# Kernel tuning notes

Measured on AMD Instinct MI355X. Metric: run time of the kernel, lower is better.

Reference implementation:

```python
import jax, jax.numpy as jnp
import numpy as np

N = 8192
F_DIM = 512
H_DIM = 256


def _xavier(key, shape):
    fan_in, fan_out = shape
    limit = float(np.sqrt(6.0 / (fan_in + fan_out)))
    return jax.random.uniform(key, shape, jnp.float32, -limit, limit)


def setup_inputs() -> dict:
    key = jax.random.key(0)
    k1, k2, k3, k4, k5, k6, k7 = jax.random.split(key, 7)
    inp = {
        "input": jax.random.normal(k1, (N, F_DIM), jnp.float32),
        "wavelets": jax.random.normal(k2, (N, N), jnp.float32) / np.sqrt(N),
        "wavelets_inv": jax.random.normal(k3, (N, N), jnp.float32) / np.sqrt(N),
        "W1": _xavier(k4, (F_DIM, H_DIM)),
        "W2": _xavier(k5, (H_DIM, H_DIM)),
        "filter1": jax.random.uniform(k6, (N,), jnp.float32, 0.9, 1.1),
        "filter2": jax.random.uniform(k7, (N,), jnp.float32, 0.9, 1.1),
    }
    return inp


def _gwnn_layer(x, wavelets, wavelets_inv, weight, filt):
    # torch: wavelets @ diag(filt) @ (wavelets_inv @ (x @ W))
    # diag(filt) right-multiply == column-wise scale of wavelets (same math,
    # avoids the O(N^3) dense diag matmul).
    t = x @ weight                      # [N, C_out]
    s = wavelets_inv @ t                # [N, C_out] (spectral domain)
    return (wavelets * filt[None, :]) @ s  # [N, C_out]


def reference(input, wavelets, wavelets_inv, W1, W2, filter1, filter2):
    # eval mode: dropout is identity
    h1 = jax.nn.relu(_gwnn_layer(input, wavelets, wavelets_inv, W1, filter1))
    out = _gwnn_layer(h1, wavelets, wavelets_inv, W2, filter2)
    return out
```

## Files before the change

kernel.cpp:

```cpp
#include <hip/hip_runtime.h>
#include <hip/hip_bf16.h>

using f32x4 = __attribute__((ext_vector_type(4))) float;
using s16x8 = __attribute__((ext_vector_type(8))) short;

#define DEVFN static __device__ __forceinline__

static constexpr int NCOL = 256;
static constexpr int MROWS = 8192;
static constexpr int BM = 64;
static constexpr int BK = 128;
static constexpr int THREADS = 512;
static constexpr int NTILE = MROWS / BM;

DEVFN unsigned short f2bf(float f) {
  union { float f; unsigned u; } x; x.f = f;
  unsigned u = x.u;
  u += 0x7fffu + ((u >> 16) & 1u);
  return (unsigned short)(u >> 16);
}

DEVFN s16x8 pack8(f32x4 v0, f32x4 v1) {
  union { s16x8 v; __hip_bfloat162 h[4]; } pk;
  pk.h[0] = __float22bfloat162_rn(float2{v0[0], v0[1]});
  pk.h[1] = __float22bfloat162_rn(float2{v0[2], v0[3]});
  pk.h[2] = __float22bfloat162_rn(float2{v1[0], v1[1]});
  pk.h[3] = __float22bfloat162_rn(float2{v1[2], v1[3]});
  return pk.v;
}

DEVFN void async16(void* lds, const void* g) {
  __builtin_amdgcn_global_load_lds((const __attribute__((address_space(1))) unsigned*)g,
                                   (__attribute__((address_space(3))) unsigned*)lds,
                                   16, 0, 0);
}

template<bool ABLK, int KS, bool WB>
__global__ __launch_bounds__(THREADS, 4)
void gemm_m(const void* __restrict__ Aany, int Kfull,
            const unsigned short* __restrict__ Bp8,
            float* __restrict__ Cpart, unsigned short* __restrict__ Awb)
{
  __shared__ __align__(16) unsigned short As[2][BM * BK];

  const int nwg = NTILE * KS, q = nwg / 8;
  const int logical = (blockIdx.x & 7) * q + (blockIdx.x >> 3);
  const int kh = logical >> 7;
  const int tile = logical & 127;
  const int klen = Kfull / KS;
  const int nt = klen / BK;
  const int k0 = kh * klen;
  const int tid = threadIdx.x, lane = tid & 63;
  const int wm = (tid >> 6) >> 2;
  const int wn = (tid >> 6) & 3;
  const int lr = lane & 15, lg = lane >> 4;
  const int srow = tid >> 3, sseg = tid & 7;

  const float* Af32 = (const float*)Aany;
  const unsigned short* Abf = (const unsigned short*)Aany;
  const int ktiles = Kfull >> 7;

  f32x4 rv[4];
  auto loadA = [&](int t) {
    const float* p = Af32 + (size_t)(tile * BM + srow) * Kfull + k0 + t * BK + sseg * 16;
    rv[0] = *(const f32x4*)p;       rv[1] = *(const f32x4*)(p + 4);
    rv[2] = *(const f32x4*)(p + 8); rv[3] = *(const f32x4*)(p + 12);
  };
  auto putA = [&](int buf, int t) {
    s16x8 p0 = pack8(rv[0], rv[1]), p1 = pack8(rv[2], rv[3]);
    const int kc0 = sseg * 2;
    *(s16x8*)&As[buf][srow * 128 + (((kc0    ) ^ (srow & 15)) << 3)] = p0;
    *(s16x8*)&As[buf][srow * 128 + (((kc0 + 1) ^ (srow & 15)) << 3)] = p1;
    if constexpr (WB) {
      unsigned short* w = Awb + ((size_t)tile * ktiles + (k0 >> 7) + t) * 8192
                        + srow * 128 + sseg * 16;
      *(s16x8*)w = p0; *(s16x8*)(w + 8) = p1;
    }
  };
  auto stageBf = [&](int buf, int t) {
    const unsigned short* base = Abf + ((size_t)tile * ktiles + (k0 >> 7) + t) * 8192;
#pragma unroll
    for (int o = 0; o < 2; ++o) {
      const int bs = o * 8192 + tid * 16;
      const int row = bs >> 8, ch = (bs >> 4) & 15;
      async16(&As[buf][o * 4096 + tid * 8], base + row * 128 + ((ch ^ (row & 15)) << 3));
    }
  };

  const unsigned short* bptr = Bp8 + ((size_t)(k0 >> 3) + lg) * 2048
                             + (size_t)(wn * 64 + lr) * 8;
  s16x8 bb[2][4];
  auto ldb = [&](const unsigned short* p, s16x8* d) {
#pragma unroll
    for (int fn = 0; fn < 4; ++fn) d[fn] = *(const s16x8*)(p + fn * 128);
  };

  f32x4 acc[2][4] = {};

  if constexpr (ABLK) { stageBf(0, 0); } else { loadA(0); putA(0, 0); }
  ldb(bptr, bb[0]);
  bptr += 8192;
  __syncthreads();

  int cur = 0;
  for (int t = 0; t < nt; ++t) {
    const bool pre = (t + 1 < nt);
    if (pre) { if constexpr (ABLK) stageBf(cur ^ 1, t + 1); else loadA(t + 1); }
#pragma unroll
    for (int s = 0; s < 4; ++s) {
      if (pre || s < 3) { ldb(bptr, bb[(s + 1) & 1]); bptr += 8192; }
      s16x8 a0, a1;
      {
        const int r0 = wm * 32 + lr, kc = s * 4 + lg;
        a0 = *(const s16x8*)&As[cur][r0 * 128 + ((kc ^ (r0 & 15)) << 3)];
        const int r1 = r0 + 16;
        a1 = *(const s16x8*)&As[cur][r1 * 128 + ((kc ^ (r1 & 15)) << 3)];
      }
#pragma unroll
      for (int fn = 0; fn < 4; ++fn) {
        acc[0][fn] = __builtin_amdgcn_mfma_f32_16x16x32_bf16(a0, bb[s & 1][fn], acc[0][fn], 0, 0, 0);
        acc[1][fn] = __builtin_amdgcn_mfma_f32_16x16x32_bf16(a1, bb[s & 1][fn], acc[1][fn], 0, 0, 0);
      }
    }
    if constexpr (!ABLK) { if (pre) putA(cur ^ 1, t + 1); }
    __syncthreads();
    cur ^= 1;
  }

  float* Co = Cpart + (size_t)kh * MROWS * NCOL;
#pragma unroll
  for (int fm = 0; fm < 2; ++fm) {
    const int row = tile * BM + wm * 32 + fm * 16 + lg * 4;
#pragma unroll
    for (int fn = 0; fn < 4; ++fn) {
      const int col = wn * 64 + fn * 16 + lr;
#pragma unroll
      for (int r = 0; r < 4; ++r)
        Co[(size_t)(row + r) * NCOL + col] = acc[fm][fn][r];
    }
  }
}


__global__ void k_convert_p8(const float* __restrict__ W, int K,
                             unsigned short* __restrict__ outp) {
  int tid = blockIdx.x * blockDim.x + threadIdx.x;
  if (tid >= K * NCOL / 4) return;
  int j = tid & (NCOL - 1);
  int i0 = (tid >> 8) << 2;
  unsigned short u[4];
#pragma unroll
  for (int r = 0; r < 4; ++r) u[r] = f2bf(W[(size_t)(i0 + r) * NCOL + j]);
  size_t off = ((size_t)(i0 >> 3) * NCOL + j) * 8 + (i0 & 7);
  *(ushort4*)&outp[off] = make_ushort4(u[0], u[1], u[2], u[3]);
}

template<int NS, int MODE>
__global__ void k_reduce(const float* __restrict__ P, const float* __restrict__ filt,
                         void* __restrict__ Out) {
  int tid = blockIdx.x * blockDim.x + threadIdx.x;
  if constexpr (MODE == 0) {
    int j = tid & (NCOL - 1);
    int i0 = (tid >> 8) << 2;
    unsigned short u[4];
#pragma unroll
    for (int r = 0; r < 4; ++r) {
      size_t o = (size_t)(i0 + r) * NCOL + j;
      float v = 0.f;
#pragma unroll
      for (int h = 0; h < NS; ++h) v += P[(size_t)h * MROWS * NCOL + o];
      if (filt) v *= filt[i0 + r];
      u[r] = f2bf(v);
    }
    size_t off = ((size_t)(i0 >> 3) * NCOL + j) * 8 + (i0 & 7);
    *(ushort4*)&((unsigned short*)Out)[off] = make_ushort4(u[0], u[1], u[2], u[3]);
  } else {
    size_t o = (size_t)tid * 4;
    float4 v = *(const float4*)&P[o];
#pragma unroll
    for (int h = 1; h < NS; ++h) {
      float4 b = *(const float4*)&P[(size_t)h * MROWS * NCOL + o];
      v.x += b.x; v.y += b.y; v.z += b.z; v.w += b.w;
    }
    if constexpr (MODE == 1) {
      const int m = (int)(o >> 8), c = (int)(o & 255);
      ushort4 u;
      u.x = f2bf(fmaxf(v.x, 0.f)); u.y = f2bf(fmaxf(v.y, 0.f));
      u.z = f2bf(fmaxf(v.z, 0.f)); u.w = f2bf(fmaxf(v.w, 0.f));
      size_t off = ((size_t)(m >> 6) * 2 + (c >> 7)) * 8192 + (m & 63) * 128 + (c & 127);
      *(ushort4*)&((unsigned short*)Out)[off] = u;
    } else {
      *(float4*)&((float*)Out)[o] = v;
    }
  }
}

extern "C" void kernel_launch(void* const* d_in, const int* in_sizes, int n_in,
                              void* d_out, int out_size, void* d_ws, size_t ws_size,
                              hipStream_t stream) {
  const float* input = (const float*)d_in[0];
  const float* Wv    = (const float*)d_in[1];
  const float* Winv  = (const float*)d_in[2];
  const float* W1    = (const float*)d_in[3];
  const float* W2    = (const float*)d_in[4];
  const float* f1    = (const float*)d_in[5];
  const float* f2    = (const float*)d_in[6];
  float* out = (float*)d_out;

  char* ws = (char*)d_ws;
  unsigned short* WvB   = (unsigned short*)(ws);
  unsigned short* WinvB = (unsigned short*)(ws + 0x8000000);
  float* part           = (float*)(ws + 0x10000000);
  unsigned short* t1p   = (unsigned short*)(ws + 0x12000000);
  unsigned short* s1p   = (unsigned short*)(ws + 0x12400000);
  unsigned short* t2p   = (unsigned short*)(ws + 0x12800000);
  unsigned short* s2p   = (unsigned short*)(ws + 0x12C00000);
  unsigned short* h1b   = (unsigned short*)(ws + 0x13000000);
  unsigned short* W1p   = (unsigned short*)(ws + 0x13400000);
  unsigned short* W2p   = (unsigned short*)(ws + 0x13440000);

  dim3 gT(THREADS);
  dim3 g4(NTILE * 4), g2(NTILE * 2);
  dim3 rT(256), rG(MROWS * NCOL / 4 / 256);

  k_convert_p8<<<dim3(128), rT, 0, stream>>>(W1, 512, W1p);
  k_convert_p8<<<dim3(64),  rT, 0, stream>>>(W2, 256, W2p);

  gemm_m<false, 4, false><<<g4, gT, 0, stream>>>((const void*)input, 512, W1p, part, nullptr);
  k_reduce<4, 0><<<rG, rT, 0, stream>>>(part, nullptr, t1p);
  gemm_m<false, 4, true><<<g4, gT, 0, stream>>>((const void*)Winv, 8192, t1p, part, WinvB);
  k_reduce<4, 0><<<rG, rT, 0, stream>>>(part, f1, s1p);
  gemm_m<false, 4, true><<<g4, gT, 0, stream>>>((const void*)Wv, 8192, s1p, part, WvB);
  k_reduce<4, 1><<<rG, rT, 0, stream>>>(part, nullptr, h1b);
  gemm_m<true, 2, false><<<g2, gT, 0, stream>>>((const void*)h1b, 256, W2p, part, nullptr);
  k_reduce<2, 0><<<rG, rT, 0, stream>>>(part, nullptr, t2p);
  gemm_m<true, 4, false><<<g4, gT, 0, stream>>>((const void*)WinvB, 8192, t2p, part, nullptr);
  k_reduce<4, 0><<<rG, rT, 0, stream>>>(part, f2, s2p);
  gemm_m<true, 4, false><<<g4, gT, 0, stream>>>((const void*)WvB, 8192, s2p, part, nullptr);
  k_reduce<4, 2><<<rG, rT, 0, stream>>>(part, nullptr, out);
}
```

Measured before the change: 430.2 us.

## Double K tile depth to 256 and split fp32 A staging in halves

Raises the GEMM K tile from 128 to 256, so each block does twice as many MFMA steps per barrier and the LDS swizzle widens to 32 chunks. The fp32 A path now loads and converts in two halves interleaved with the MFMA steps, which keeps register pressure down and overlaps the global loads with compute. The blocked bf16 layouts for the cached wavelets and h1 change to 256-wide tiles, and the small W1/W2 GEMMs use fewer K splits. LDS use doubles to 64KB per block, which may cut occupancy.

Result: slower. 497.2 us (+15.6%).

```diff
diff --git a/kernel.cpp b/kernel.cpp
--- a/kernel.cpp
+++ b/kernel.cpp
@@ -9,7 +9,7 @@
 static constexpr int NCOL = 256;
 static constexpr int MROWS = 8192;
 static constexpr int BM = 64;
-static constexpr int BK = 128;
+static constexpr int BK = 256;
 static constexpr int THREADS = 512;
 static constexpr int NTILE = MROWS / BM;
 
@@ -58,32 +58,34 @@
 
   const float* Af32 = (const float*)Aany;
   const unsigned short* Abf = (const unsigned short*)Aany;
-  const int ktiles = Kfull >> 7;
+  const int ktiles = Kfull >> 8;
 
   f32x4 rv[4];
-  auto loadA = [&](int t) {
-    const float* p = Af32 + (size_t)(tile * BM + srow) * Kfull + k0 + t * BK + sseg * 16;
+  auto loadA_h = [&](int t, int h) {
+    const float* p = Af32 + (size_t)(tile * BM + srow) * Kfull
+                   + k0 + t * BK + sseg * 32 + h * 16;
     rv[0] = *(const f32x4*)p;       rv[1] = *(const f32x4*)(p + 4);
     rv[2] = *(const f32x4*)(p + 8); rv[3] = *(const f32x4*)(p + 12);
   };
-  auto putA = [&](int buf, int t) {
+  auto putA_h = [&](int buf, int t, int h) {
     s16x8 p0 = pack8(rv[0], rv[1]), p1 = pack8(rv[2], rv[3]);
-    const int kc0 = sseg * 2;
-    *(s16x8*)&As[buf][srow * 128 + (((kc0    ) ^ (srow & 15)) << 3)] = p0;
-    *(s16x8*)&As[buf][srow * 128 + (((kc0 + 1) ^ (srow & 15)) << 3)] = p1;
+    const int c0 = sseg * 4 + h * 2;
+    *(s16x8*)&As[buf][srow * 256 + (((c0    ) ^ (srow & 31)) << 3)] = p0;
+    *(s16x8*)&As[buf][srow * 256 + (((c0 + 1) ^ (srow & 31)) << 3)] = p1;
     if constexpr (WB) {
-      unsigned short* w = Awb + ((size_t)tile * ktiles + (k0 >> 7) + t) * 8192
-                        + srow * 128 + sseg * 16;
+      unsigned short* w = Awb + ((size_t)tile * ktiles + (k0 >> 8) + t) * 16384
+                        + srow * 256 + sseg * 32 + h * 16;
       *(s16x8*)w = p0; *(s16x8*)(w + 8) = p1;
     }
   };
   auto stageBf = [&](int buf, int t) {
-    const unsigned short* base = Abf + ((size_t)tile * ktiles + (k0 >> 7) + t) * 8192;
-#pragma unroll
-    for (int o = 0; o < 2; ++o) {
-      const int bs = o * 8192 + tid * 16;
-      const int row = bs >> 8, ch = (bs >> 4) & 15;
-      async16(&As[buf][o * 4096 + tid * 8], base + row * 128 + ((ch ^ (row & 15)) << 3));
+    const unsigned short* base = Abf + ((size_t)tile * ktiles + (k0 >> 8) + t) * 16384;
+#pragma unroll
+    for (int o = 0; o < 4; ++o) {
+      const int slot = o * 8192 + tid * 16;
+      const int row = slot >> 9, ch = (slot >> 4) & 31;
+      async16(&As[buf][o * 4096 + tid * 8],
+              base + row * 256 + ((ch ^ (row & 31)) << 3));
     }
   };
 
@@ -97,32 +99,39 @@
 
   f32x4 acc[2][4] = {};
 
-  if constexpr (ABLK) { stageBf(0, 0); } else { loadA(0); putA(0, 0); }
-  ldb(bptr, bb[0]);
-  bptr += 8192;
+  if constexpr (ABLK) {
+    stageBf(0, 0);
+  } else {
+    loadA_h(0, 0); putA_h(0, 0, 0);
+    loadA_h(0, 1); putA_h(0, 0, 1);
+  }
+  ldb(bptr, bb[0]); bptr += 8192;
   __syncthreads();
 
   int cur = 0;
   for (int t = 0; t < nt; ++t) {
     const bool pre = (t + 1 < nt);
-    if (pre) { if constexpr (ABLK) stageBf(cur ^ 1, t + 1); else loadA(t + 1); }
-#pragma unroll
-    for (int s = 0; s < 4; ++s) {
-      if (pre || s < 3) { ldb(bptr, bb[(s + 1) & 1]); bptr += 8192; }
+    if (pre) { if constexpr (ABLK) stageBf(cur ^ 1, t + 1); else loadA_h(t + 1, 0); }
+#pragma unroll
+    for (int s = 0; s < 8; ++s) {
+      if (s < 7 || pre) { ldb(bptr, bb[(s + 1) & 1]); bptr += 8192; }
       s16x8 a0, a1;
       {
         const int r0 = wm * 32 + lr, kc = s * 4 + lg;
-        a0 = *(const s16x8*)&As[cur][r0 * 128 + ((kc ^ (r0 & 15)) << 3)];
+        a0 = *(const s16x8*)&As[cur][r0 * 256 + ((kc ^ (r0 & 31)) << 3)];
         const int r1 = r0 + 16;
-        a1 = *(const s16x8*)&As[cur][r1 * 128 + ((kc ^ (r1 & 15)) << 3)];
+        a1 = *(const s16x8*)&As[cur][r1 * 256 + ((kc ^ (r1 & 31)) << 3)];
       }
 #pragma unroll
       for (int fn = 0; fn < 4; ++fn) {
         acc[0][fn] = __builtin_amdgcn_mfma_f32_16x16x32_bf16(a0, bb[s & 1][fn], acc[0][fn], 0, 0, 0);
         acc[1][fn] = __builtin_amdgcn_mfma_f32_16x16x32_bf16(a1, bb[s & 1][fn], acc[1][fn], 0, 0, 0);
       }
-    }
-    if constexpr (!ABLK) { if (pre) putA(cur ^ 1, t + 1); }
+      if constexpr (!ABLK) {
+        if (pre && s == 3) { putA_h(cur ^ 1, t + 1, 0); loadA_h(t + 1, 1); }
+        if (pre && s == 6) { putA_h(cur ^ 1, t + 1, 1); }
+      }
+    }
     __syncthreads();
     cur ^= 1;
   }
@@ -187,7 +196,7 @@
       ushort4 u;
       u.x = f2bf(fmaxf(v.x, 0.f)); u.y = f2bf(fmaxf(v.y, 0.f));
       u.z = f2bf(fmaxf(v.z, 0.f)); u.w = f2bf(fmaxf(v.w, 0.f));
-      size_t off = ((size_t)(m >> 6) * 2 + (c >> 7)) * 8192 + (m & 63) * 128 + (c & 127);
+      size_t off = (size_t)(m >> 6) * 16384 + (m & 63) * 256 + c;
       *(ushort4*)&((unsigned short*)Out)[off] = u;
     } else {
       *(float4*)&((float*)Out)[o] = v;
@@ -220,20 +229,20 @@
   unsigned short* W2p   = (unsigned short*)(ws + 0x13440000);
 
   dim3 gT(THREADS);
-  dim3 g4(NTILE * 4), g2(NTILE * 2);
+  dim3 g4(NTILE * 4), g2(NTILE * 2), g1(NTILE);
   dim3 rT(256), rG(MROWS * NCOL / 4 / 256);
 
   k_convert_p8<<<dim3(128), rT, 0, stream>>>(W1, 512, W1p);
   k_convert_p8<<<dim3(64),  rT, 0, stream>>>(W2, 256, W2p);
 
-  gemm_m<false, 4, false><<<g4, gT, 0, stream>>>((const void*)input, 512, W1p, part, nullptr);
-  k_reduce<4, 0><<<rG, rT, 0, stream>>>(part, nullptr, t1p);
+  gemm_m<false, 2, false><<<g2, gT, 0, stream>>>((const void*)input, 512, W1p, part, nullptr);
+  k_reduce<2, 0><<<rG, rT, 0, stream>>>(part, nullptr, t1p);
   gemm_m<false, 4, true><<<g4, gT, 0, stream>>>((const void*)Winv, 8192, t1p, part, WinvB);
   k_reduce<4, 0><<<rG, rT, 0, stream>>>(part, f1, s1p);
   gemm_m<false, 4, true><<<g4, gT, 0, stream>>>((const void*)Wv, 8192, s1p, part, WvB);
   k_reduce<4, 1><<<rG, rT, 0, stream>>>(part, nullptr, h1b);
-  gemm_m<true, 2, false><<<g2, gT, 0, stream>>>((const void*)h1b, 256, W2p, part, nullptr);
-  k_reduce<2, 0><<<rG, rT, 0, stream>>>(part, nullptr, t2p);
+  gemm_m<true, 1, false><<<g1, gT, 0, stream>>>((const void*)h1b, 256, W2p, part, nullptr);
+  k_reduce<1, 0><<<rG, rT, 0, stream>>>(part, nullptr, t2p);
   gemm_m<true, 4, false><<<g4, gT, 0, stream>>>((const void*)WinvB, 8192, t2p, part, nullptr);
   k_reduce<4, 0><<<rG, rT, 0, stream>>>(part, f2, s2p);
   gemm_m<true, 4, false><<<g4, gT, 0, stream>>>((const void*)WvB, 8192, s2p, part, nullptr);
```

## Pre-convert A matrices to blocked bf16 and stage B through LDS asynchronously

Applied to the files above, without the earlier changes.

Adds dedicated conversion kernels that turn Wv, Winv and the input into swizzled 64x64 bf16 blocks before any GEMM, so every GEMM streams bf16 A tiles with async global-to-LDS loads. B tiles are now also staged into LDS asynchronously instead of being read per-wave from global into registers, and BK drops to 64. The small GEMMs (x@W1, h1@W2) run without K-split and write packed bf16 output directly, which removes two reduce launches. The cost is two extra full passes over the 8192x8192 matrices as standalone conversions, where before the conversion was fused into the first GEMMs that read them, plus a larger LDS footprint that may reduce occupancy.

Result: faster. 410.8 us (-4.5%).

```diff
diff --git a/kernel.cpp b/kernel.cpp
--- a/kernel.cpp
+++ b/kernel.cpp
@@ -9,7 +9,7 @@
 static constexpr int NCOL = 256;
 static constexpr int MROWS = 8192;
 static constexpr int BM = 64;
-static constexpr int BK = 128;
+static constexpr int BK = 64;
 static constexpr int THREADS = 512;
 static constexpr int NTILE = MROWS / BM;
 
@@ -35,112 +35,107 @@
                                    16, 0, 0);
 }
 
-template<bool ABLK, int KS, bool WB>
+
+template<int KS, int EPI>
 __global__ __launch_bounds__(THREADS, 4)
-void gemm_m(const void* __restrict__ Aany, int Kfull,
+void gemm_b(const unsigned short* __restrict__ Ablk, int Kfull,
             const unsigned short* __restrict__ Bp8,
-            float* __restrict__ Cpart, unsigned short* __restrict__ Awb)
+            float* __restrict__ Cpart, unsigned short* __restrict__ Pout)
 {
   __shared__ __align__(16) unsigned short As[2][BM * BK];
+  __shared__ __align__(16) unsigned short Bs[2][BK * NCOL];
 
   const int nwg = NTILE * KS, q = nwg / 8;
   const int logical = (blockIdx.x & 7) * q + (blockIdx.x >> 3);
-  const int kh = logical >> 7;
-  const int tile = logical & 127;
+  const int kh = logical / NTILE;
+  const int tile = logical % NTILE;
   const int klen = Kfull / KS;
   const int nt = klen / BK;
   const int k0 = kh * klen;
+  const int KT = Kfull >> 6;
   const int tid = threadIdx.x, lane = tid & 63;
   const int wm = (tid >> 6) >> 2;
   const int wn = (tid >> 6) & 3;
   const int lr = lane & 15, lg = lane >> 4;
-  const int srow = tid >> 3, sseg = tid & 7;
-
-  const float* Af32 = (const float*)Aany;
-  const unsigned short* Abf = (const unsigned short*)Aany;
-  const int ktiles = Kfull >> 7;
-
-  f32x4 rv[4];
-  auto loadA = [&](int t) {
-    const float* p = Af32 + (size_t)(tile * BM + srow) * Kfull + k0 + t * BK + sseg * 16;
-    rv[0] = *(const f32x4*)p;       rv[1] = *(const f32x4*)(p + 4);
-    rv[2] = *(const f32x4*)(p + 8); rv[3] = *(const f32x4*)(p + 12);
+
+  auto stage = [&](int buf, int t) {
+    const unsigned short* asrc = Ablk + ((size_t)tile * KT + (k0 >> 6) + t) * 4096 + tid * 8;
+    async16(&As[buf][tid * 8], asrc);
+    const unsigned short* bsrc = Bp8 + (size_t)(k0 + t * BK) * NCOL + tid * 8;
+#pragma unroll
+    for (int o = 0; o < 4; ++o)
+      async16(&Bs[buf][o * 4096 + tid * 8], bsrc + o * 4096);
   };
-  auto putA = [&](int buf, int t) {
-    s16x8 p0 = pack8(rv[0], rv[1]), p1 = pack8(rv[2], rv[3]);
-    const int kc0 = sseg * 2;
-    *(s16x8*)&As[buf][srow * 128 + (((kc0    ) ^ (srow & 15)) << 3)] = p0;
-    *(s16x8*)&As[buf][srow * 128 + (((kc0 + 1) ^ (srow & 15)) << 3)] = p1;
-    if constexpr (WB) {
-      unsigned short* w = Awb + ((size_t)tile * ktiles + (k0 >> 7) + t) * 8192
-                        + srow * 128 + sseg * 16;
-      *(s16x8*)w = p0; *(s16x8*)(w + 8) = p1;
-    }
-  };
-  auto stageBf = [&](int buf, int t) {
-    const unsigned short* base = Abf + ((size_t)tile * ktiles + (k0 >> 7) + t) * 8192;
-#pragma unroll
-    for (int o = 0; o < 2; ++o) {
-      const int bs = o * 8192 + tid * 16;
-      const int row = bs >> 8, ch = (bs >> 4) & 15;
-      async16(&As[buf][o * 4096 + tid * 8], base + row * 128 + ((ch ^ (row & 15)) << 3));
-    }
-  };
-
-  const unsigned short* bptr = Bp8 + ((size_t)(k0 >> 3) + lg) * 2048
-                             + (size_t)(wn * 64 + lr) * 8;
-  s16x8 bb[2][4];
-  auto ldb = [&](const unsigned short* p, s16x8* d) {
-#pragma unroll
-    for (int fn = 0; fn < 4; ++fn) d[fn] = *(const s16x8*)(p + fn * 128);
-  };
 
   f32x4 acc[2][4] = {};
 
-  if constexpr (ABLK) { stageBf(0, 0); } else { loadA(0); putA(0, 0); }
-  ldb(bptr, bb[0]);
-  bptr += 8192;
+  stage(0, 0);
   __syncthreads();
 
   int cur = 0;
   for (int t = 0; t < nt; ++t) {
-    const bool pre = (t + 1 < nt);
-    if (pre) { if constexpr (ABLK) stageBf(cur ^ 1, t + 1); else loadA(t + 1); }
-#pragma unroll
-    for (int s = 0; s < 4; ++s) {
-      if (pre || s < 3) { ldb(bptr, bb[(s + 1) & 1]); bptr += 8192; }
-      s16x8 a0, a1;
-      {
-        const int r0 = wm * 32 + lr, kc = s * 4 + lg;
-        a0 = *(const s16x8*)&As[cur][r0 * 128 + ((kc ^ (r0 & 15)) << 3)];
-        const int r1 = r0 + 16;
-        a1 = *(const s16x8*)&As[cur][r1 * 128 + ((kc ^ (r1 & 15)) << 3)];
+    if (t + 1 < nt) stage(cur ^ 1, t + 1);
+#pragma unroll
+    for (int s = 0; s < 2; ++s) {
+      const int kc = s * 4 + lg;
+      const int r0 = wm * 32 + lr, r1 = r0 + 16;
+      s16x8 a0 = *(const s16x8*)&As[cur][r0 * 64 + ((kc ^ (r0 & 7)) << 3)];
+      s16x8 a1 = *(const s16x8*)&As[cur][r1 * 64 + ((kc ^ (r1 & 7)) << 3)];
+#pragma unroll
+      for (int fn = 0; fn < 4; ++fn) {
+        s16x8 b = *(const s16x8*)&Bs[cur][kc * 2048 + (wn * 64 + fn * 16 + lr) * 8];
+        acc[0][fn] = __builtin_amdgcn_mfma_f32_16x16x32_bf16(a0, b, acc[0][fn], 0, 0, 0);
+        acc[1][fn] = __builtin_amdgcn_mfma_f32_16x16x32_bf16(a1, b, acc[1][fn], 0, 0, 0);
       }
-#pragma unroll
-      for (int fn = 0; fn < 4; ++fn) {
-        acc[0][fn] = __builtin_amdgcn_mfma_f32_16x16x32_bf16(a0, bb[s & 1][fn], acc[0][fn], 0, 0, 0);
-        acc[1][fn] = __builtin_amdgcn_mfma_f32_16x16x32_bf16(a1, bb[s & 1][fn], acc[1][fn], 0, 0, 0);
-      }
-    }
-    if constexpr (!ABLK) { if (pre) putA(cur ^ 1, t + 1); }
+    }
     __syncthreads();
     cur ^= 1;
   }
 
-  float* Co = Cpart + (size_t)kh * MROWS * NCOL;
-#pragma unroll
-  for (int fm = 0; fm < 2; ++fm) {
-    const int row = tile * BM + wm * 32 + fm * 16 + lg * 4;
-#pragma unroll
-    for (int fn = 0; fn < 4; ++fn) {
-      const int col = wn * 64 + fn * 16 + lr;
-#pragma unroll
-      for (int r = 0; r < 4; ++r)
-        Co[(size_t)(row + r) * NCOL + col] = acc[fm][fn][r];
+  if constexpr (EPI == 0) {
+    float* Co = Cpart + (size_t)kh * MROWS * NCOL;
+#pragma unroll
+    for (int fm = 0; fm < 2; ++fm) {
+      const int row = tile * BM + wm * 32 + fm * 16 + lg * 4;
+#pragma unroll
+      for (int fn = 0; fn < 4; ++fn) {
+        const int col = wn * 64 + fn * 16 + lr;
+#pragma unroll
+        for (int r = 0; r < 4; ++r)
+          Co[(size_t)(row + r) * NCOL + col] = acc[fm][fn][r];
+      }
+    }
+  } else {
+#pragma unroll
+    for (int fm = 0; fm < 2; ++fm) {
+      const int r0 = tile * BM + wm * 32 + fm * 16 + lg * 4;
+#pragma unroll
+      for (int fn = 0; fn < 4; ++fn) {
+        const int col = wn * 64 + fn * 16 + lr;
+        ushort4 u;
+        u.x = f2bf(acc[fm][fn][0]); u.y = f2bf(acc[fm][fn][1]);
+        u.z = f2bf(acc[fm][fn][2]); u.w = f2bf(acc[fm][fn][3]);
+        *(ushort4*)&Pout[((size_t)(r0 >> 3) * 256 + col) * 8 + (r0 & 7)] = u;
+      }
     }
   }
 }
 
+
+template<int KTSH>
+__global__ void k_cvt_ablk(const float* __restrict__ W, unsigned short* __restrict__ outp) {
+  const int K = 64 << KTSH;
+  size_t gid = (size_t)blockIdx.x * blockDim.x + threadIdx.x;
+  const int k8 = (int)(gid & 7);
+  const size_t rr = gid >> 3;
+  const int row = (int)(rr & 63);
+  const size_t bt = rr >> 6;
+  const int t = (int)(bt & ((1 << KTSH) - 1));
+  const size_t T = bt >> KTSH;
+  const float* p = W + (T * 64 + row) * (size_t)K + t * 64 + k8 * 8;
+  s16x8 v = pack8(*(const f32x4*)p, *(const f32x4*)(p + 4));
+  *(s16x8*)&outp[bt * 4096 + row * 64 + ((k8 ^ (row & 7)) << 3)] = v;
+}
 
 __global__ void k_convert_p8(const float* __restrict__ W, int K,
                              unsigned short* __restrict__ outp) {
@@ -155,7 +150,7 @@
   *(ushort4*)&outp[off] = make_ushort4(u[0], u[1], u[2], u[3]);
 }
 
-template<int NS, int MODE>
+template<int MODE>
 __global__ void k_reduce(const float* __restrict__ P, const float* __restrict__ filt,
                          void* __restrict__ Out) {
   int tid = blockIdx.x * blockDim.x + threadIdx.x;
@@ -166,9 +161,8 @@
 #pragma unroll
     for (int r = 0; r < 4; ++r) {
       size_t o = (size_t)(i0 + r) * NCOL + j;
-      float v = 0.f;
-#pragma unroll
-      for (int h = 0; h < NS; ++h) v += P[(size_t)h * MROWS * NCOL + o];
+      float v = P[o] + P[(size_t)MROWS * NCOL + o]
+              + P[2 * (size_t)MROWS * NCOL + o] + P[3 * (size_t)MROWS * NCOL + o];
       if (filt) v *= filt[i0 + r];
       u[r] = f2bf(v);
     }
@@ -176,18 +170,19 @@
     *(ushort4*)&((unsigned short*)Out)[off] = make_ushort4(u[0], u[1], u[2], u[3]);
   } else {
     size_t o = (size_t)tid * 4;
-    float4 v = *(const float4*)&P[o];
-#pragma unroll
-    for (int h = 1; h < NS; ++h) {
-      float4 b = *(const float4*)&P[(size_t)h * MROWS * NCOL + o];
-      v.x += b.x; v.y += b.y; v.z += b.z; v.w += b.w;
-    }
+    float4 a = *(const float4*)&P[o];
+    float4 b = *(const float4*)&P[(size_t)MROWS * NCOL + o];
+    float4 c = *(const float4*)&P[2 * (size_t)MROWS * NCOL + o];
+    float4 d = *(const float4*)&P[3 * (size_t)MROWS * NCOL + o];
+    float4 v; v.x = a.x + b.x + c.x + d.x; v.y = a.y + b.y + c.y + d.y;
+    v.z = a.z + b.z + c.z + d.z; v.w = a.w + b.w + c.w + d.w;
     if constexpr (MODE == 1) {
-      const int m = (int)(o >> 8), c = (int)(o & 255);
+      const int m = (int)(o >> 8), c0 = (int)(o & 255);
       ushort4 u;
       u.x = f2bf(fmaxf(v.x, 0.f)); u.y = f2bf(fmaxf(v.y, 0.f));
       u.z = f2bf(fmaxf(v.z, 0.f)); u.w = f2bf(fmaxf(v.w, 0.f));
-      size_t off = ((size_t)(m >> 6) * 2 + (c >> 7)) * 8192 + (m & 63) * 128 + (c & 127);
+      size_t off = (((size_t)(m >> 6) * 4 + (c0 >> 6)) * 4096)
+                 + (m & 63) * 64 + ((((c0 >> 3) & 7) ^ (m & 7)) << 3) + (c0 & 7);
       *(ushort4*)&((unsigned short*)Out)[off] = u;
     } else {
       *(float4*)&((float*)Out)[o] = v;
@@ -210,32 +205,34 @@
   char* ws = (char*)d_ws;
   unsigned short* WvB   = (unsigned short*)(ws);
   unsigned short* WinvB = (unsigned short*)(ws + 0x8000000);
-  float* part           = (float*)(ws + 0x10000000);
-  unsigned short* t1p   = (unsigned short*)(ws + 0x12000000);
-  unsigned short* s1p   = (unsigned short*)(ws + 0x12400000);
-  unsigned short* t2p   = (unsigned short*)(ws + 0x12800000);
-  unsigned short* s2p   = (unsigned short*)(ws + 0x12C00000);
-  unsigned short* h1b   = (unsigned short*)(ws + 0x13000000);
-  unsigned short* W1p   = (unsigned short*)(ws + 0x13400000);
-  unsigned short* W2p   = (unsigned short*)(ws + 0x13440000);
+  unsigned short* inB   = (unsigned short*)(ws + 0x10000000);
+  float* part           = (float*)(ws + 0x10800000);
+  unsigned short* t1p   = (unsigned short*)(ws + 0x12800000);
+  unsigned short* s1p   = (unsigned short*)(ws + 0x12C00000);
+  unsigned short* t2p   = (unsigned short*)(ws + 0x13000000);
+  unsigned short* s2p   = (unsigned short*)(ws + 0x13400000);
+  unsigned short* h1b   = (unsigned short*)(ws + 0x13800000);
+  unsigned short* W1p   = (unsigned short*)(ws + 0x13C00000);
+  unsigned short* W2p   = (unsigned short*)(ws + 0x13C40000);
 
   dim3 gT(THREADS);
-  dim3 g4(NTILE * 4), g2(NTILE * 2);
+  dim3 g4(NTILE * 4), g1(NTILE);
   dim3 rT(256), rG(MROWS * NCOL / 4 / 256);
 
+  k_cvt_ablk<7><<<dim3(32768), rT, 0, stream>>>(Wv, WvB);
+  k_cvt_ablk<7><<<dim3(32768), rT, 0, stream>>>(Winv, WinvB);
+  k_cvt_ablk<3><<<dim3(2048),  rT, 0, stream>>>(input, inB);
   k_convert_p8<<<dim3(128), rT, 0, stream>>>(W1, 512, W1p);
   k_convert_p8<<<dim3(64),  rT, 0, stream>>>(W2, 256, W2p);
 
-  gemm_m<false, 4, false><<<g4, gT, 0, stream>>>((const void*)input, 512, W1p, part, nullptr);
-  k_reduce<4, 0><<<rG, rT, 0, stream>>>(part, nullptr, t1p);
-  gemm_m<false, 4, true><<<g4, gT, 0, stream>>>((const void*)Winv, 8192, t1p, part, WinvB);
-  k_reduce<4, 0><<<rG, rT, 0, stream>>>(part, f1, s1p);
-  gemm_m<false, 4, true><<<g4, gT, 0, stream>>>((const void*)Wv, 8192, s1p, part, WvB);
-  k_reduce<4, 1><<<rG, rT, 0, stream>>>(part, nullptr, h1b);
-  gemm_m<true, 2, false><<<g2, gT, 0, stream>>>((const void*)h1b, 256, W2p, part, nullptr);
-  k_reduce<2, 0><<<rG, rT, 0, stream>>>(part, nullptr, t2p);
-  gemm_m<true, 4, false><<<g4, gT, 0, stream>>>((const void*)WinvB, 8192, t2p, part, nullptr);
-  k_reduce<4, 0><<<rG, rT, 0, stream>>>(part, f2, s2p);
-  gemm_m<true, 4, false><<<g4, gT, 0, stream>>>((const void*)WvB, 8192, s2p, part, nullptr);
-  k_reduce<4, 2><<<rG, rT, 0, stream>>>(part, nullptr, out);
-}
+  gemm_b<1, 1><<<g1, gT, 0, stream>>>(inB, 512, W1p, nullptr, t1p);
+  gemm_b<4, 0><<<g4, gT, 0, stream>>>(WinvB, 8192, t1p, part, nullptr);
+  k_reduce<0><<<rG, rT, 0, stream>>>(part, f1, s1p);
+  gemm_b<4, 0><<<g4, gT, 0, stream>>>(WvB, 8192, s1p, part, nullptr);
+  k_reduce<1><<<rG, rT, 0, stream>>>(part, nullptr, h1b);
+  gemm_b<1, 1><<<g1, gT, 0, stream>>>(h1b, 256, W2p, nullptr, t2p);
+  gemm_b<4, 0><<<g4, gT, 0, stream>>>(WinvB, 8192, t2p, part, nullptr);
+  k_reduce<0><<<rG, rT, 0, stream>>>(part, f2, s2p);
+  gemm_b<4, 0><<<g4, gT, 0, stream>>>(WvB, 8192, s2p, part, nullptr);
+  k_reduce<2><<<rG, rT, 0, stream>>>(part, nullptr, out);
+}
```
